# Optimization experiments

Hardware: AMD Instinct MI355X
Metric: run time of the kernel (lower is better)

The kernel has to match this reference:

```python
import jax, jax.numpy as jnp
import numpy as np

WEIGHT = 1.0  # init kwarg 'weight'


def _histc(x, bins):
    """torch.histc semantics: bins over [x.min(), x.max()], rightmost bin inclusive."""
    mn, mx = x.min(), x.max()
    w = (mx - mn) / bins
    safe_w = jnp.where(w > 0, w, 1.0)
    b = jnp.clip(jnp.floor((x - mn) / safe_w), 0, bins - 1).astype(jnp.int32)
    return jnp.zeros((bins,), jnp.float32).at[b].add(1.0)


def setup_inputs() -> dict:
    key = jax.random.key(0)
    k1, k2, k3 = jax.random.split(key, 3)
    C, H, W = 64, 128, 128
    inp = jax.random.normal(k1, (1, C, H, W), jnp.float32)
    match = jax.random.normal(k2, (1, C, H, W), jnp.float32)
    mask_tight = (jax.random.uniform(k3, (1, 1, H, W)) > 0.3).astype(jnp.float32)
    return {"input": inp, "match": match, "mask_tight": mask_tight, "bins": 256}


def reference(input, match, mask_tight, bins):
    C = input.shape[1]
    # --- compute_histogram (torch.histc per channel of masked match) ---
    mm = (match * mask_tight).reshape(C, -1)
    style_his = jax.lax.stop_gradient(jax.vmap(lambda v: _histc(v, bins))(mm))  # (C, bins)

    # --- remap_histogram ---
    x = (input * mask_tight).reshape(C, -1)  # (C, N)
    N = x.shape[1]
    channel_min = x.min(1, keepdims=True)  # (C,1)
    channel_max = x.max(1, keepdims=True)  # (C,1)
    step = (channel_max - channel_min) / bins
    rng = jnp.arange(1, N + 1, dtype=x.dtype)[None, :]  # (1, N) ranks 1..N

    sh = style_his * N / style_his.sum(1, keepdims=True)
    cdf = jnp.cumsum(sh, axis=1)                                  # (C, bins)
    cdf_prev = jnp.concatenate([jnp.zeros((C, 1), cdf.dtype), cdf[:, :-1]], axis=1)

    # CDF inversion: count bins whose cdf < rank  -> idx in [0, bins]
    idx = jnp.sum(cdf[:, None, :] - rng[:, :, None] < 0, axis=2).astype(jnp.int32)  # (C, N)

    # Faithful select_idx: gather from FLATTENED hist with un-offset bin indices
    flat_idx = idx.reshape(-1)
    sel = lambda h: h.reshape(-1)[flat_idx].reshape(C, N)

    ratio = jnp.clip((rng - sel(cdf_prev)) / (1e-8 + sel(cdf)), 0.0, 1.0)  # (C, N)
    input_corr = channel_min + (ratio + idx) * step
    input_corr = input_corr.at[:, -1].set(channel_max[:, 0])
    input_corr = sel(input_corr)  # faithful final flattened re-gather

    # --- loss (scalar stored as self.loss in the torch module) ---
    loss = jnp.mean((input_corr - x) ** 2)
    loss = loss * mask_tight.sum() * C / input.size * WEIGHT
    return loss
```

## Files before the change

### kernel.cpp

```cpp
#include <hip/hip_runtime.h>
#include <math.h>

#define C_CH  64
#define HW    16384
#define BINS  256

#define WS_CDF   0
#define WS_XMN   (C_CH * BINS)
#define WS_XMX   (WS_XMN + 1)
#define WS_MSUM  (WS_XMN + 2)
#define WS_SSE   (WS_XMN + 3)
#define WS_CNT   (WS_XMN + 4)

__device__ inline float4 ld4(const float* p) { return *(const float4*)p; }

__device__ inline int lbound(const float* a, float rank) {
    int lo = 0, hi = BINS;
    while (lo < hi) { int mid = (lo + hi) >> 1; if (a[mid] < rank) lo = mid + 1; else hi = mid; }
    return (lo > 255) ? 255 : lo;
}

__global__ __launch_bounds__(1024, 4) void k1_hist(const float* __restrict__ input,
                                                   const float* __restrict__ match,
                                                   const float* __restrict__ mask,
                                                   float* __restrict__ ws) {
    const int b = blockIdx.x, tid = threadIdx.x;
    const int wave = tid >> 6, lane = tid & 63;
    __shared__ float wmin[16], wmax[16], wsum[16];
    __shared__ int hist[BINS];

    if (b < C_CH) {
        const float* m = match + b * HW;

        float v[16];
        float mn = INFINITY, mx = -INFINITY;
        #pragma unroll
        for (int k = 0; k < 4; k++) {
            float4 mv = ld4(m + k * 4096 + 4 * tid);
            float4 kv = ld4(mask + k * 4096 + 4 * tid);
            v[4 * k + 0] = mv.x * kv.x; v[4 * k + 1] = mv.y * kv.y;
            v[4 * k + 2] = mv.z * kv.z; v[4 * k + 3] = mv.w * kv.w;
            #pragma unroll
            for (int j = 0; j < 4; j++) {
                mn = fminf(mn, v[4 * k + j]);
                mx = fmaxf(mx, v[4 * k + j]);
            }
        }
        #pragma unroll
        for (int s = 32; s > 0; s >>= 1) {
            mn = fminf(mn, __shfl_xor(mn, s, 64));
            mx = fmaxf(mx, __shfl_xor(mx, s, 64));
        }
        if (lane == 0) { wmin[wave] = mn; wmax[wave] = mx; }
        if (tid < BINS) hist[tid] = 0;
        __syncthreads();
        mn = wmin[0]; mx = wmax[0];
        #pragma unroll
        for (int j = 1; j < 16; j++) { mn = fminf(mn, wmin[j]); mx = fmaxf(mx, wmax[j]); }

        float w  = (mx - mn) * (1.0f / 256.0f);
        float sw = (w > 0.0f) ? w : 1.0f;

        int zc = 0;
        #pragma unroll
        for (int j = 0; j < 16; j++) {
            if (v[j] == 0.0f) { zc++; }
            else {
                float bb = floorf((v[j] - mn) / sw);
                bb = fminf(fmaxf(bb, 0.0f), 255.0f);
                atomicAdd(&hist[(int)bb], 1);
            }
        }
        #pragma unroll
        for (int s = 32; s > 0; s >>= 1) zc += __shfl_xor(zc, s, 64);
        if (lane == 0) wsum[wave] = (float)zc;
        __syncthreads();
        if (tid == 0) {
            int z = 0;
            #pragma unroll
            for (int j = 0; j < 16; j++) z += (int)wsum[j];
            float bb = floorf((0.0f - mn) / sw);
            bb = fminf(fmaxf(bb, 0.0f), 255.0f);
            hist[(int)bb] += z;
        }
        __syncthreads();

        if (wave == 0) {
            int h0 = hist[4 * lane], h1 = hist[4 * lane + 1];
            int h2 = hist[4 * lane + 2], h3 = hist[4 * lane + 3];
            int p1 = h0 + h1, p2 = p1 + h2, s4 = p2 + h3;
            int sc = s4;
            #pragma unroll
            for (int off = 1; off < 64; off <<= 1) {
                int t = __shfl_up(sc, off, 64);
                if (lane >= off) sc += t;
            }
            int e = sc - s4;
            float4 o = make_float4((float)(e + h0), (float)(e + p1),
                                   (float)(e + p2), (float)(e + s4));
            *(float4*)&ws[WS_CDF + b * BINS + 4 * lane] = o;
        }
    } else {
        float xmn = INFINITY, xmx = -INFINITY, msum = 0.0f;
        #pragma unroll
        for (int k = 0; k < 4; k++) {
            float4 xv = ld4(input + k * 4096 + 4 * tid);
            float4 kv = ld4(mask + k * 4096 + 4 * tid);
            float v0 = xv.x * kv.x, v1 = xv.y * kv.y, v2 = xv.z * kv.z, v3 = xv.w * kv.w;
            xmn = fminf(xmn, fminf(fminf(v0, v1), fminf(v2, v3)));
            xmx = fmaxf(xmx, fmaxf(fmaxf(v0, v1), fmaxf(v2, v3)));
            msum += kv.x + kv.y + kv.z + kv.w;
        }
        #pragma unroll
        for (int s = 32; s > 0; s >>= 1) {
            xmn = fminf(xmn, __shfl_xor(xmn, s, 64));
            xmx = fmaxf(xmx, __shfl_xor(xmx, s, 64));
            msum += __shfl_xor(msum, s, 64);
        }
        if (lane == 0) { wmin[wave] = xmn; wmax[wave] = xmx; wsum[wave] = msum; }
        __syncthreads();
        if (tid == 0) {
            #pragma unroll
            for (int j = 1; j < 16; j++) {
                xmn = fminf(xmn, wmin[j]);
                xmx = fmaxf(xmx, wmax[j]);
            }
            float ms = 0.0f;
            #pragma unroll
            for (int j = 0; j < 16; j++) ms += wsum[j];
            ws[WS_XMN] = xmn;
            ws[WS_XMX] = xmx;
            ws[WS_MSUM] = ms;
            ws[WS_SSE] = 0.0f;
            ((int*)ws)[WS_CNT] = 0;
        }
    }
}

__global__ __launch_bounds__(256) void k2_loss(const float* __restrict__ input,
                                               const float* __restrict__ mask,
                                               float* __restrict__ ws,
                                               float* __restrict__ out) {
    const int c = blockIdx.x >> 2;
    const int base = (blockIdx.x & 3) * 4096;
    const int tid = threadIdx.x;
    const int wave = tid >> 6, lane = tid & 63;

    __shared__ float scdf[BINS], sc0[BINS], sT[BINS], red[4];
    scdf[tid] = ws[WS_CDF + c * BINS + tid];
    sc0[tid]  = ws[WS_CDF + tid];
    __syncthreads();

    {
        const float xmn = ws[WS_XMN], xmx = ws[WS_XMX];
        float step = (xmx - xmn) * (1.0f / 256.0f);
        float rank = (float)(tid + 1);
        int idx = lbound(sc0, rank);
        float cp = (idx > 0) ? sc0[idx - 1] : 0.0f;
        float cc = sc0[idx];
        float ratio = fminf(fmaxf((rank - cp) / (1e-8f + cc), 0.0f), 1.0f);
        sT[tid] = xmn + (ratio + (float)idx) * step;
    }
    __syncthreads();

    const float* x  = input + c * HW + base;
    const float* mk = mask + base;

    float acc = 0.0f;
    int lo = lbound(scdf, (float)(base + 4 * tid + 1));
    #pragma unroll
    for (int k = 0; k < 4; k++) {
        float4 xv = ld4(x + k * 1024 + 4 * tid);
        float4 kv = ld4(mk + k * 1024 + 4 * tid);
        float v[4] = { xv.x * kv.x, xv.y * kv.y, xv.z * kv.z, xv.w * kv.w };
        float rank0 = (float)(base + k * 1024 + 4 * tid + 1);
        #pragma unroll
        for (int j = 0; j < 4; j++) {
            float rnk = rank0 + (float)j;
            while (scdf[lo] < rnk) lo++;
            float d = sT[lo] - v[j];
            acc += d * d;
        }
    }

    #pragma unroll
    for (int s = 32; s > 0; s >>= 1) acc += __shfl_xor(acc, s, 64);
    if (lane == 0) red[wave] = acc;
    __syncthreads();

    if (tid == 0) {
        float ssum = red[0] + red[1] + red[2] + red[3];
        atomicAdd(&ws[WS_SSE], ssum);
        __threadfence();
        int old = atomicAdd(&((int*)ws)[WS_CNT], 1);
        if (old == gridDim.x - 1) {
            float sse  = atomicAdd(&ws[WS_SSE], 0.0f);
            float msum = ws[WS_MSUM];
            double mean = (double)sse / (double)(C_CH * HW);
            out[0] = (float)(mean * (double)msum * (double)C_CH / (double)(C_CH * HW));
        }
    }
}

extern "C" void kernel_launch(void* const* d_in, const int* in_sizes, int n_in,
                              void* d_out, int out_size, void* d_ws, size_t ws_size,
                              hipStream_t stream) {
    const float* input = (const float*)d_in[0];
    const float* match = (const float*)d_in[1];
    const float* mask  = (const float*)d_in[2];
    float* ws          = (float*)d_ws;
    float* out         = (float*)d_out;

    k1_hist<<<C_CH + 1, 1024, 0, stream>>>(input, match, mask, ws);
    k2_loss<<<C_CH * 4, 256,  0, stream>>>(input, mask, ws, out);
}
```

Measured before the change: 78.91 us.

## Fuse histogram and loss kernels into one persistent kernel with grid barriers

Merges the two launches into a single 256-block kernel. Each block loads its quarter-channel slice of match, input and mask once and keeps the values in registers across phases. Software grid barriers synchronise the phases: partial min/max exchange, a per-block shared histogram merged into global with atomics, then CDF building and the loss. This removes a kernel launch and the second read of input, and spreads the histogram over four times more blocks. In exchange it relies on all 256 blocks being co-resident for the spin barriers and adds global atomic traffic.

```diff
diff --git a/kernel.cpp b/kernel.cpp
--- a/kernel.cpp
+++ b/kernel.cpp
@@ -4,15 +4,42 @@
 #define C_CH  64
 #define HW    16384
 #define BINS  256
-
-#define WS_CDF   0
-#define WS_XMN   (C_CH * BINS)
-#define WS_XMX   (WS_XMN + 1)
-#define WS_MSUM  (WS_XMN + 2)
-#define WS_SSE   (WS_XMN + 3)
-#define WS_CNT   (WS_XMN + 4)
+#define NBLK  256
+#define QHW   4096
+
+#define WS_HIST  0
+#define WS_PMIN  (C_CH * BINS)
+#define WS_PMAX  (WS_PMIN + C_CH * 4)
+#define WS_IPMN  (WS_PMAX + C_CH * 4)
+#define WS_IPMX  (WS_IPMN + 4)
+#define WS_MSUM  (WS_IPMX + 4)
+#define WS_SSE   (WS_MSUM + 4)
+#define WS_CNT   (WS_SSE + 1)
+
+__device__ unsigned g_bar_cnt = 0;
+__device__ unsigned g_bar_gen = 0;
 
 __device__ inline float4 ld4(const float* p) { return *(const float4*)p; }
+__device__ inline float aldf(float* p) { return atomicAdd(p, 0.0f); }
+__device__ inline int   aldi(int* p)   { return atomicAdd(p, 0); }
+
+__device__ inline void gridbar() {
+    __syncthreads();
+    if (threadIdx.x == 0) {
+        __threadfence();
+        unsigned g = __hip_atomic_load(&g_bar_gen, __ATOMIC_RELAXED, __HIP_MEMORY_SCOPE_AGENT);
+        if (atomicAdd(&g_bar_cnt, 1u) == NBLK - 1u) {
+            atomicExch(&g_bar_cnt, 0u);
+            __threadfence();
+            atomicAdd(&g_bar_gen, 1u);
+        } else {
+            while (__hip_atomic_load(&g_bar_gen, __ATOMIC_RELAXED, __HIP_MEMORY_SCOPE_AGENT) == g)
+                __builtin_amdgcn_s_sleep(1);
+        }
+        __threadfence();
+    }
+    __syncthreads();
+}
 
 __device__ inline int lbound(const float* a, float rank) {
     int lo = 0, hi = BINS;
@@ -20,184 +47,200 @@
     return (lo > 255) ? 255 : lo;
 }
 
-__global__ __launch_bounds__(1024, 4) void k1_hist(const float* __restrict__ input,
-                                                   const float* __restrict__ match,
-                                                   const float* __restrict__ mask,
-                                                   float* __restrict__ ws) {
-    const int b = blockIdx.x, tid = threadIdx.x;
+__global__ __launch_bounds__(256) void fused(const float* __restrict__ input,
+                                             const float* __restrict__ match,
+                                             const float* __restrict__ mask,
+                                             float* __restrict__ ws,
+                                             float* __restrict__ out) {
+    const int blk = blockIdx.x, tid = threadIdx.x;
+    const int c = blk >> 2, q = blk & 3, base = q * QHW;
     const int wave = tid >> 6, lane = tid & 63;
-    __shared__ float wmin[16], wmax[16], wsum[16];
-    __shared__ int hist[BINS];
-
-    if (b < C_CH) {
-        const float* m = match + b * HW;
-
-        float v[16];
-        float mn = INFINITY, mx = -INFINITY;
-        #pragma unroll
-        for (int k = 0; k < 4; k++) {
-            float4 mv = ld4(m + k * 4096 + 4 * tid);
-            float4 kv = ld4(mask + k * 4096 + 4 * tid);
-            v[4 * k + 0] = mv.x * kv.x; v[4 * k + 1] = mv.y * kv.y;
-            v[4 * k + 2] = mv.z * kv.z; v[4 * k + 3] = mv.w * kv.w;
+    int* iws = (int*)ws;
+
+    __shared__ int   hist[BINS];
+    __shared__ int   shc[BINS], sh0[BINS];
+    __shared__ float scdf[BINS], sc0[BINS], sT[BINS];
+    __shared__ float wr_a[4], wr_b[4], wr_c[4], wr_d[4], wr_e[4];
+    __shared__ float s_mn, s_mx, s_xmn, s_xmx;
+
+    const float* m  = match + c * HW + base;
+    const float* x  = input + c * HW + base;
+    const float* mk = mask + base;
+
+    float vm[16], vx[16];
+    float mn = INFINITY, mx = -INFINITY;
+    float xmn = INFINITY, xmx = -INFINITY, msum = 0.0f;
+    #pragma unroll
+    for (int k = 0; k < 4; k++) {
+        float4 mv = ld4(m  + k * 1024 + 4 * tid);
+        float4 kv = ld4(mk + k * 1024 + 4 * tid);
+        float4 xv = ld4(x  + k * 1024 + 4 * tid);
+        vm[4*k+0] = mv.x * kv.x; vm[4*k+1] = mv.y * kv.y;
+        vm[4*k+2] = mv.z * kv.z; vm[4*k+3] = mv.w * kv.w;
+        vx[4*k+0] = xv.x * kv.x; vx[4*k+1] = xv.y * kv.y;
+        vx[4*k+2] = xv.z * kv.z; vx[4*k+3] = xv.w * kv.w;
+        #pragma unroll
+        for (int j = 0; j < 4; j++) {
+            mn = fminf(mn, vm[4*k+j]);
+            mx = fmaxf(mx, vm[4*k+j]);
+        }
+        if (c == 0) {
             #pragma unroll
             for (int j = 0; j < 4; j++) {
-                mn = fminf(mn, v[4 * k + j]);
-                mx = fmaxf(mx, v[4 * k + j]);
+                xmn = fminf(xmn, vx[4*k+j]);
+                xmx = fmaxf(xmx, vx[4*k+j]);
             }
-        }
-        #pragma unroll
-        for (int s = 32; s > 0; s >>= 1) {
-            mn = fminf(mn, __shfl_xor(mn, s, 64));
-            mx = fmaxf(mx, __shfl_xor(mx, s, 64));
-        }
-        if (lane == 0) { wmin[wave] = mn; wmax[wave] = mx; }
-        if (tid < BINS) hist[tid] = 0;
-        __syncthreads();
-        mn = wmin[0]; mx = wmax[0];
-        #pragma unroll
-        for (int j = 1; j < 16; j++) { mn = fminf(mn, wmin[j]); mx = fmaxf(mx, wmax[j]); }
-
-        float w  = (mx - mn) * (1.0f / 256.0f);
-        float sw = (w > 0.0f) ? w : 1.0f;
-
-        int zc = 0;
-        #pragma unroll
-        for (int j = 0; j < 16; j++) {
-            if (v[j] == 0.0f) { zc++; }
-            else {
-                float bb = floorf((v[j] - mn) / sw);
-                bb = fminf(fmaxf(bb, 0.0f), 255.0f);
-                atomicAdd(&hist[(int)bb], 1);
-            }
-        }
-        #pragma unroll
-        for (int s = 32; s > 0; s >>= 1) zc += __shfl_xor(zc, s, 64);
-        if (lane == 0) wsum[wave] = (float)zc;
-        __syncthreads();
-        if (tid == 0) {
-            int z = 0;
-            #pragma unroll
-            for (int j = 0; j < 16; j++) z += (int)wsum[j];
-            float bb = floorf((0.0f - mn) / sw);
-            bb = fminf(fmaxf(bb, 0.0f), 255.0f);
-            hist[(int)bb] += z;
-        }
-        __syncthreads();
-
-        if (wave == 0) {
-            int h0 = hist[4 * lane], h1 = hist[4 * lane + 1];
-            int h2 = hist[4 * lane + 2], h3 = hist[4 * lane + 3];
-            int p1 = h0 + h1, p2 = p1 + h2, s4 = p2 + h3;
-            int sc = s4;
-            #pragma unroll
-            for (int off = 1; off < 64; off <<= 1) {
-                int t = __shfl_up(sc, off, 64);
-                if (lane >= off) sc += t;
-            }
-            int e = sc - s4;
-            float4 o = make_float4((float)(e + h0), (float)(e + p1),
-                                   (float)(e + p2), (float)(e + s4));
-            *(float4*)&ws[WS_CDF + b * BINS + 4 * lane] = o;
-        }
-    } else {
-        float xmn = INFINITY, xmx = -INFINITY, msum = 0.0f;
-        #pragma unroll
-        for (int k = 0; k < 4; k++) {
-            float4 xv = ld4(input + k * 4096 + 4 * tid);
-            float4 kv = ld4(mask + k * 4096 + 4 * tid);
-            float v0 = xv.x * kv.x, v1 = xv.y * kv.y, v2 = xv.z * kv.z, v3 = xv.w * kv.w;
-            xmn = fminf(xmn, fminf(fminf(v0, v1), fminf(v2, v3)));
-            xmx = fmaxf(xmx, fmaxf(fmaxf(v0, v1), fmaxf(v2, v3)));
             msum += kv.x + kv.y + kv.z + kv.w;
         }
+    }
+    #pragma unroll
+    for (int s = 32; s > 0; s >>= 1) {
+        mn = fminf(mn, __shfl_xor(mn, s, 64));
+        mx = fmaxf(mx, __shfl_xor(mx, s, 64));
+    }
+    if (c == 0) {
         #pragma unroll
         for (int s = 32; s > 0; s >>= 1) {
             xmn = fminf(xmn, __shfl_xor(xmn, s, 64));
             xmx = fmaxf(xmx, __shfl_xor(xmx, s, 64));
             msum += __shfl_xor(msum, s, 64);
         }
-        if (lane == 0) { wmin[wave] = xmn; wmax[wave] = xmx; wsum[wave] = msum; }
-        __syncthreads();
-        if (tid == 0) {
-            #pragma unroll
-            for (int j = 1; j < 16; j++) {
-                xmn = fminf(xmn, wmin[j]);
-                xmx = fmaxf(xmx, wmax[j]);
-            }
-            float ms = 0.0f;
-            #pragma unroll
-            for (int j = 0; j < 16; j++) ms += wsum[j];
-            ws[WS_XMN] = xmn;
-            ws[WS_XMX] = xmx;
-            ws[WS_MSUM] = ms;
-            ws[WS_SSE] = 0.0f;
-            ((int*)ws)[WS_CNT] = 0;
-        }
-    }
-}
-
-__global__ __launch_bounds__(256) void k2_loss(const float* __restrict__ input,
-                                               const float* __restrict__ mask,
-                                               float* __restrict__ ws,
-                                               float* __restrict__ out) {
-    const int c = blockIdx.x >> 2;
-    const int base = (blockIdx.x & 3) * 4096;
-    const int tid = threadIdx.x;
-    const int wave = tid >> 6, lane = tid & 63;
-
-    __shared__ float scdf[BINS], sc0[BINS], sT[BINS], red[4];
-    scdf[tid] = ws[WS_CDF + c * BINS + tid];
-    sc0[tid]  = ws[WS_CDF + tid];
+    }
+    if (lane == 0) {
+        wr_a[wave] = mn; wr_b[wave] = mx;
+        if (c == 0) { wr_c[wave] = msum; wr_d[wave] = xmn; wr_e[wave] = xmx; }
+    }
+    if (q == 0) atomicExch(&iws[WS_HIST + c * BINS + tid], 0);
+    if (blk == 0 && tid == 0) { atomicExch(&ws[WS_SSE], 0.0f); atomicExch(&iws[WS_CNT], 0); }
+    __syncthreads();
+    if (tid == 0) {
+        float a = wr_a[0], b = wr_b[0];
+        #pragma unroll
+        for (int j = 1; j < 4; j++) { a = fminf(a, wr_a[j]); b = fmaxf(b, wr_b[j]); }
+        atomicExch(&ws[WS_PMIN + c * 4 + q], a);
+        atomicExch(&ws[WS_PMAX + c * 4 + q], b);
+        if (c == 0) {
+            float ms  = wr_c[0] + wr_c[1] + wr_c[2] + wr_c[3];
+            float ixn = fminf(fminf(wr_d[0], wr_d[1]), fminf(wr_d[2], wr_d[3]));
+            float ixx = fmaxf(fmaxf(wr_e[0], wr_e[1]), fmaxf(wr_e[2], wr_e[3]));
+            atomicExch(&ws[WS_MSUM + q], ms);
+            atomicExch(&ws[WS_IPMN + q], ixn);
+            atomicExch(&ws[WS_IPMX + q], ixx);
+        }
+    }
+    gridbar();
+
+    if (tid == 0) {
+        float a = aldf(&ws[WS_PMIN + c * 4 + 0]);
+        float b = aldf(&ws[WS_PMAX + c * 4 + 0]);
+        #pragma unroll
+        for (int j = 1; j < 4; j++) {
+            a = fminf(a, aldf(&ws[WS_PMIN + c * 4 + j]));
+            b = fmaxf(b, aldf(&ws[WS_PMAX + c * 4 + j]));
+        }
+        s_mn = a; s_mx = b;
+    }
+    hist[tid] = 0;
+    __syncthreads();
+    mn = s_mn; mx = s_mx;
+
+    float w  = (mx - mn) * (1.0f / 256.0f);
+    float sw = (w > 0.0f) ? w : 1.0f;
+
+    int zc = 0;
+    #pragma unroll
+    for (int j = 0; j < 16; j++) {
+        if (vm[j] == 0.0f) { zc++; }
+        else {
+            float bb = floorf((vm[j] - mn) / sw);
+            bb = fminf(fmaxf(bb, 0.0f), 255.0f);
+            atomicAdd(&hist[(int)bb], 1);
+        }
+    }
+    #pragma unroll
+    for (int s = 32; s > 0; s >>= 1) zc += __shfl_xor(zc, s, 64);
+    if (lane == 0) wr_a[wave] = (float)zc;
+    __syncthreads();
+    if (tid == 0) {
+        int z = (int)wr_a[0] + (int)wr_a[1] + (int)wr_a[2] + (int)wr_a[3];
+        float bb = floorf((0.0f - mn) / sw);
+        bb = fminf(fmaxf(bb, 0.0f), 255.0f);
+        hist[(int)bb] += z;
+    }
+    __syncthreads();
+    atomicAdd(&iws[WS_HIST + c * BINS + tid], hist[tid]);
+    gridbar();
+
+    shc[tid] = aldi(&iws[WS_HIST + c * BINS + tid]);
+    sh0[tid] = (c == 0) ? shc[tid] : aldi(&iws[WS_HIST + tid]);
+    __syncthreads();
+    if (wave < 2) {
+        const int* hsrc = wave ? sh0 : shc;
+        float* dst = wave ? sc0 : scdf;
+        int h0 = hsrc[4*lane], h1 = hsrc[4*lane+1], h2 = hsrc[4*lane+2], h3 = hsrc[4*lane+3];
+        int p1 = h0 + h1, p2 = p1 + h2, s4 = p2 + h3;
+        int sc = s4;
+        #pragma unroll
+        for (int off = 1; off < 64; off <<= 1) {
+            int t = __shfl_up(sc, off, 64);
+            if (lane >= off) sc += t;
+        }
+        int e = sc - s4;
+        *(float4*)&dst[4*lane] = make_float4((float)(e + h0), (float)(e + p1),
+                                             (float)(e + p2), (float)(e + s4));
+    }
+    if (tid == 128) {
+        float a = aldf(&ws[WS_IPMN + 0]);
+        float b = aldf(&ws[WS_IPMX + 0]);
+        #pragma unroll
+        for (int j = 1; j < 4; j++) {
+            a = fminf(a, aldf(&ws[WS_IPMN + j]));
+            b = fmaxf(b, aldf(&ws[WS_IPMX + j]));
+        }
+        s_xmn = a; s_xmx = b;
+    }
     __syncthreads();
 
     {
-        const float xmn = ws[WS_XMN], xmx = ws[WS_XMX];
-        float step = (xmx - xmn) * (1.0f / 256.0f);
+        float step = (s_xmx - s_xmn) * (1.0f / 256.0f);
         float rank = (float)(tid + 1);
         int idx = lbound(sc0, rank);
         float cp = (idx > 0) ? sc0[idx - 1] : 0.0f;
         float cc = sc0[idx];
         float ratio = fminf(fmaxf((rank - cp) / (1e-8f + cc), 0.0f), 1.0f);
-        sT[tid] = xmn + (ratio + (float)idx) * step;
-    }
-    __syncthreads();
-
-    const float* x  = input + c * HW + base;
-    const float* mk = mask + base;
+        sT[tid] = s_xmn + (ratio + (float)idx) * step;
+    }
+    __syncthreads();
 
     float acc = 0.0f;
     int lo = lbound(scdf, (float)(base + 4 * tid + 1));
     #pragma unroll
     for (int k = 0; k < 4; k++) {
-        float4 xv = ld4(x + k * 1024 + 4 * tid);
-        float4 kv = ld4(mk + k * 1024 + 4 * tid);
-        float v[4] = { xv.x * kv.x, xv.y * kv.y, xv.z * kv.z, xv.w * kv.w };
         float rank0 = (float)(base + k * 1024 + 4 * tid + 1);
         #pragma unroll
         for (int j = 0; j < 4; j++) {
             float rnk = rank0 + (float)j;
             while (scdf[lo] < rnk) lo++;
-            float d = sT[lo] - v[j];
+            float d = sT[lo] - vx[4 * k + j];
             acc += d * d;
         }
     }
-
     #pragma unroll
     for (int s = 32; s > 0; s >>= 1) acc += __shfl_xor(acc, s, 64);
-    if (lane == 0) red[wave] = acc;
-    __syncthreads();
-
-    if (tid == 0) {
-        float ssum = red[0] + red[1] + red[2] + red[3];
+    if (lane == 0) wr_b[wave] = acc;
+    __syncthreads();
+
+    if (tid == 0) {
+        float ssum = wr_b[0] + wr_b[1] + wr_b[2] + wr_b[3];
         atomicAdd(&ws[WS_SSE], ssum);
         __threadfence();
-        int old = atomicAdd(&((int*)ws)[WS_CNT], 1);
-        if (old == gridDim.x - 1) {
-            float sse  = atomicAdd(&ws[WS_SSE], 0.0f);
-            float msum = ws[WS_MSUM];
+        int old = atomicAdd(&iws[WS_CNT], 1);
+        if (old == NBLK - 1) {
+            float sse = aldf(&ws[WS_SSE]);
+            float ms2 = aldf(&ws[WS_MSUM + 0]) + aldf(&ws[WS_MSUM + 1]) +
+                        aldf(&ws[WS_MSUM + 2]) + aldf(&ws[WS_MSUM + 3]);
             double mean = (double)sse / (double)(C_CH * HW);
-            out[0] = (float)(mean * (double)msum * (double)C_CH / (double)(C_CH * HW));
+            out[0] = (float)(mean * (double)ms2 * (double)C_CH / (double)(C_CH * HW));
         }
     }
 }
@@ -211,6 +254,5 @@
     float* ws          = (float*)d_ws;
     float* out         = (float*)d_out;
 
-    k1_hist<<<C_CH + 1, 1024, 0, stream>>>(input, match, mask, ws);
-    k2_loss<<<C_CH * 4, 256,  0, stream>>>(input, mask, ws, out);
-}
+    fused<<<NBLK, 256, 0, stream>>>(input, match, mask, ws, out);
+}
```

After: 142.3 us. 1.8x slower.

## Split histogram pipeline into three kernels with quarter-channel blocks

Applied to the files above, without the earlier changes.

The work is now split into more, smaller blocks. A new stats kernel computes per-quarter min and max (and the input stats from channel 0) across 256 blocks. The histogram kernel then builds per-quarter partial histograms across 256 blocks. The loss kernel sums these partials, rebuilds both CDFs in every block, and runs on 512 blocks with contiguous 8-element segments per thread. The aim is to use more of the GPU's compute units than the earlier 65 blocks of 1024 threads did. The cost is one extra kernel launch, re-reading the match data, and redundant CDF scans in every loss block.

```diff
diff --git a/kernel.cpp b/kernel.cpp
--- a/kernel.cpp
+++ b/kernel.cpp
@@ -4,15 +4,23 @@
 #define C_CH  64
 #define HW    16384
 #define BINS  256
-
-#define WS_CDF   0
-#define WS_XMN   (C_CH * BINS)
-#define WS_XMX   (WS_XMN + 1)
-#define WS_MSUM  (WS_XMN + 2)
-#define WS_SSE   (WS_XMN + 3)
-#define WS_CNT   (WS_XMN + 4)
+#define QHW   4096
+#define SEG   2048
+#define NB0   256
+#define NB1   256
+#define NB2   512
+
+#define WS_H     0
+#define WS_PMIN  (NB1 * BINS)
+#define WS_PMAX  (WS_PMIN + 256)
+#define WS_IPMN  (WS_PMAX + 256)
+#define WS_IPMX  (WS_IPMN + 4)
+#define WS_MSUM  (WS_IPMX + 4)
+#define WS_SSE   (WS_MSUM + 4)
+#define WS_CNT   (WS_SSE + 1)
 
 __device__ inline float4 ld4(const float* p) { return *(const float4*)p; }
+__device__ inline float aldf(float* p) { return atomicAdd(p, 0.0f); }
 
 __device__ inline int lbound(const float* a, float rank) {
     int lo = 0, hi = BINS;
@@ -20,50 +28,98 @@
     return (lo > 255) ? 255 : lo;
 }
 
-__global__ __launch_bounds__(1024, 4) void k1_hist(const float* __restrict__ input,
-                                                   const float* __restrict__ match,
-                                                   const float* __restrict__ mask,
-                                                   float* __restrict__ ws) {
-    const int b = blockIdx.x, tid = threadIdx.x;
+__global__ __launch_bounds__(256) void k0_stats(const float* __restrict__ input,
+                                                const float* __restrict__ match,
+                                                const float* __restrict__ mask,
+                                                float* __restrict__ ws) {
+    const int blk = blockIdx.x, tid = threadIdx.x;
+    const int c = blk >> 2, q = blk & 3;
     const int wave = tid >> 6, lane = tid & 63;
-    __shared__ float wmin[16], wmax[16], wsum[16];
+    __shared__ float wa[4], wb[4], wc[4], wd[4], we[4];
+
+    const float* m  = match + c * HW + q * QHW;
+    const float* mk = mask + q * QHW;
+
+    float mn = INFINITY, mx = -INFINITY;
+    float xmn = INFINITY, xmx = -INFINITY, ms = 0.0f;
+    #pragma unroll
+    for (int k = 0; k < 4; k++) {
+        float4 mv = ld4(m  + k * 1024 + 4 * tid);
+        float4 kv = ld4(mk + k * 1024 + 4 * tid);
+        float a0 = mv.x * kv.x, a1 = mv.y * kv.y, a2 = mv.z * kv.z, a3 = mv.w * kv.w;
+        mn = fminf(mn, fminf(fminf(a0, a1), fminf(a2, a3)));
+        mx = fmaxf(mx, fmaxf(fmaxf(a0, a1), fmaxf(a2, a3)));
+    }
+    if (c == 0) {
+        const float* x = input + q * QHW;
+        #pragma unroll
+        for (int k = 0; k < 4; k++) {
+            float4 xv = ld4(x  + k * 1024 + 4 * tid);
+            float4 kv = ld4(mk + k * 1024 + 4 * tid);
+            float b0 = xv.x * kv.x, b1 = xv.y * kv.y, b2 = xv.z * kv.z, b3 = xv.w * kv.w;
+            xmn = fminf(xmn, fminf(fminf(b0, b1), fminf(b2, b3)));
+            xmx = fmaxf(xmx, fmaxf(fmaxf(b0, b1), fmaxf(b2, b3)));
+            ms += kv.x + kv.y + kv.z + kv.w;
+        }
+    }
+    #pragma unroll
+    for (int s = 32; s > 0; s >>= 1) {
+        mn = fminf(mn, __shfl_xor(mn, s, 64));
+        mx = fmaxf(mx, __shfl_xor(mx, s, 64));
+        xmn = fminf(xmn, __shfl_xor(xmn, s, 64));
+        xmx = fmaxf(xmx, __shfl_xor(xmx, s, 64));
+        ms += __shfl_xor(ms, s, 64);
+    }
+    if (lane == 0) { wa[wave] = mn; wb[wave] = mx; wc[wave] = xmn; wd[wave] = xmx; we[wave] = ms; }
+    __syncthreads();
+    if (tid == 0) {
+        float a = wa[0], b = wb[0], cmin = wc[0], cmax = wd[0], msum = we[0];
+        #pragma unroll
+        for (int j = 1; j < 4; j++) {
+            a = fminf(a, wa[j]); b = fmaxf(b, wb[j]);
+            cmin = fminf(cmin, wc[j]); cmax = fmaxf(cmax, wd[j]); msum += we[j];
+        }
+        ws[WS_PMIN + c * 4 + q] = a;
+        ws[WS_PMAX + c * 4 + q] = b;
+        if (c == 0) {
+            ws[WS_IPMN + q] = cmin;
+            ws[WS_IPMX + q] = cmax;
+            ws[WS_MSUM + q] = msum;
+            if (q == 0) { ws[WS_SSE] = 0.0f; ((int*)ws)[WS_CNT] = 0; }
+        }
+    }
+}
+
+__global__ __launch_bounds__(256) void k1_hist(const float* __restrict__ match,
+                                               const float* __restrict__ mask,
+                                               float* __restrict__ ws) {
+    const int blk = blockIdx.x, tid = threadIdx.x;
+    const int c = blk >> 2, q = blk & 3;
+    const int wave = tid >> 6, lane = tid & 63;
     __shared__ int hist[BINS];
-
-    if (b < C_CH) {
-        const float* m = match + b * HW;
-
-        float v[16];
-        float mn = INFINITY, mx = -INFINITY;
-        #pragma unroll
-        for (int k = 0; k < 4; k++) {
-            float4 mv = ld4(m + k * 4096 + 4 * tid);
-            float4 kv = ld4(mask + k * 4096 + 4 * tid);
-            v[4 * k + 0] = mv.x * kv.x; v[4 * k + 1] = mv.y * kv.y;
-            v[4 * k + 2] = mv.z * kv.z; v[4 * k + 3] = mv.w * kv.w;
-            #pragma unroll
-            for (int j = 0; j < 4; j++) {
-                mn = fminf(mn, v[4 * k + j]);
-                mx = fmaxf(mx, v[4 * k + j]);
-            }
-        }
-        #pragma unroll
-        for (int s = 32; s > 0; s >>= 1) {
-            mn = fminf(mn, __shfl_xor(mn, s, 64));
-            mx = fmaxf(mx, __shfl_xor(mx, s, 64));
-        }
-        if (lane == 0) { wmin[wave] = mn; wmax[wave] = mx; }
-        if (tid < BINS) hist[tid] = 0;
-        __syncthreads();
-        mn = wmin[0]; mx = wmax[0];
-        #pragma unroll
-        for (int j = 1; j < 16; j++) { mn = fminf(mn, wmin[j]); mx = fmaxf(mx, wmax[j]); }
-
-        float w  = (mx - mn) * (1.0f / 256.0f);
-        float sw = (w > 0.0f) ? w : 1.0f;
-
-        int zc = 0;
-        #pragma unroll
-        for (int j = 0; j < 16; j++) {
+    __shared__ float wz[4];
+
+    float mn = fminf(fminf(ws[WS_PMIN + c * 4 + 0], ws[WS_PMIN + c * 4 + 1]),
+                     fminf(ws[WS_PMIN + c * 4 + 2], ws[WS_PMIN + c * 4 + 3]));
+    float mx = fmaxf(fmaxf(ws[WS_PMAX + c * 4 + 0], ws[WS_PMAX + c * 4 + 1]),
+                     fmaxf(ws[WS_PMAX + c * 4 + 2], ws[WS_PMAX + c * 4 + 3]));
+    hist[tid] = 0;
+    __syncthreads();
+
+    float w  = (mx - mn) * (1.0f / 256.0f);
+    float sw = (w > 0.0f) ? w : 1.0f;
+
+    const float* m  = match + c * HW + q * QHW;
+    const float* mk = mask + q * QHW;
+
+    int zc = 0;
+    #pragma unroll
+    for (int k = 0; k < 4; k++) {
+        float4 mv = ld4(m  + k * 1024 + 4 * tid);
+        float4 kv = ld4(mk + k * 1024 + 4 * tid);
+        float v[4] = { mv.x * kv.x, mv.y * kv.y, mv.z * kv.z, mv.w * kv.w };
+        #pragma unroll
+        for (int j = 0; j < 4; j++) {
             if (v[j] == 0.0f) { zc++; }
             else {
                 float bb = floorf((v[j] - mn) / sw);
@@ -71,95 +127,75 @@
                 atomicAdd(&hist[(int)bb], 1);
             }
         }
-        #pragma unroll
-        for (int s = 32; s > 0; s >>= 1) zc += __shfl_xor(zc, s, 64);
-        if (lane == 0) wsum[wave] = (float)zc;
-        __syncthreads();
-        if (tid == 0) {
-            int z = 0;
-            #pragma unroll
-            for (int j = 0; j < 16; j++) z += (int)wsum[j];
-            float bb = floorf((0.0f - mn) / sw);
-            bb = fminf(fmaxf(bb, 0.0f), 255.0f);
-            hist[(int)bb] += z;
-        }
-        __syncthreads();
-
-        if (wave == 0) {
-            int h0 = hist[4 * lane], h1 = hist[4 * lane + 1];
-            int h2 = hist[4 * lane + 2], h3 = hist[4 * lane + 3];
-            int p1 = h0 + h1, p2 = p1 + h2, s4 = p2 + h3;
-            int sc = s4;
-            #pragma unroll
-            for (int off = 1; off < 64; off <<= 1) {
-                int t = __shfl_up(sc, off, 64);
-                if (lane >= off) sc += t;
-            }
-            int e = sc - s4;
-            float4 o = make_float4((float)(e + h0), (float)(e + p1),
-                                   (float)(e + p2), (float)(e + s4));
-            *(float4*)&ws[WS_CDF + b * BINS + 4 * lane] = o;
-        }
-    } else {
-        float xmn = INFINITY, xmx = -INFINITY, msum = 0.0f;
-        #pragma unroll
-        for (int k = 0; k < 4; k++) {
-            float4 xv = ld4(input + k * 4096 + 4 * tid);
-            float4 kv = ld4(mask + k * 4096 + 4 * tid);
-            float v0 = xv.x * kv.x, v1 = xv.y * kv.y, v2 = xv.z * kv.z, v3 = xv.w * kv.w;
-            xmn = fminf(xmn, fminf(fminf(v0, v1), fminf(v2, v3)));
-            xmx = fmaxf(xmx, fmaxf(fmaxf(v0, v1), fmaxf(v2, v3)));
-            msum += kv.x + kv.y + kv.z + kv.w;
-        }
-        #pragma unroll
-        for (int s = 32; s > 0; s >>= 1) {
-            xmn = fminf(xmn, __shfl_xor(xmn, s, 64));
-            xmx = fmaxf(xmx, __shfl_xor(xmx, s, 64));
-            msum += __shfl_xor(msum, s, 64);
-        }
-        if (lane == 0) { wmin[wave] = xmn; wmax[wave] = xmx; wsum[wave] = msum; }
-        __syncthreads();
-        if (tid == 0) {
-            #pragma unroll
-            for (int j = 1; j < 16; j++) {
-                xmn = fminf(xmn, wmin[j]);
-                xmx = fmaxf(xmx, wmax[j]);
-            }
-            float ms = 0.0f;
-            #pragma unroll
-            for (int j = 0; j < 16; j++) ms += wsum[j];
-            ws[WS_XMN] = xmn;
-            ws[WS_XMX] = xmx;
-            ws[WS_MSUM] = ms;
-            ws[WS_SSE] = 0.0f;
-            ((int*)ws)[WS_CNT] = 0;
-        }
-    }
+    }
+    #pragma unroll
+    for (int s = 32; s > 0; s >>= 1) zc += __shfl_xor(zc, s, 64);
+    if (lane == 0) wz[wave] = (float)zc;
+    __syncthreads();
+    if (tid == 0) {
+        int z = (int)wz[0] + (int)wz[1] + (int)wz[2] + (int)wz[3];
+        float bb = floorf((0.0f - mn) / sw);
+        bb = fminf(fmaxf(bb, 0.0f), 255.0f);
+        hist[(int)bb] += z;
+    }
+    __syncthreads();
+    ((int*)ws)[WS_H + blk * BINS + tid] = hist[tid];
 }
 
 __global__ __launch_bounds__(256) void k2_loss(const float* __restrict__ input,
                                                const float* __restrict__ mask,
                                                float* __restrict__ ws,
                                                float* __restrict__ out) {
-    const int c = blockIdx.x >> 2;
-    const int base = (blockIdx.x & 3) * 4096;
-    const int tid = threadIdx.x;
+    const int blk = blockIdx.x, tid = threadIdx.x;
+    const int c = blk >> 3, s = blk & 7, base = s * SEG;
     const int wave = tid >> 6, lane = tid & 63;
-
+    int* iws = (int*)ws;
+
+    __shared__ int   shc[BINS], sh0[BINS];
     __shared__ float scdf[BINS], sc0[BINS], sT[BINS], red[4];
-    scdf[tid] = ws[WS_CDF + c * BINS + tid];
-    sc0[tid]  = ws[WS_CDF + tid];
-    __syncthreads();
+    __shared__ float s_xmn, s_xmx;
 
     {
-        const float xmn = ws[WS_XMN], xmx = ws[WS_XMX];
-        float step = (xmx - xmn) * (1.0f / 256.0f);
+        int h = iws[WS_H + (c * 4 + 0) * BINS + tid] + iws[WS_H + (c * 4 + 1) * BINS + tid]
+              + iws[WS_H + (c * 4 + 2) * BINS + tid] + iws[WS_H + (c * 4 + 3) * BINS + tid];
+        shc[tid] = h;
+        sh0[tid] = (c == 0) ? h
+                 : iws[WS_H + 0 * BINS + tid] + iws[WS_H + 1 * BINS + tid]
+                 + iws[WS_H + 2 * BINS + tid] + iws[WS_H + 3 * BINS + tid];
+    }
+    if (tid == 0) {
+        s_xmn = fminf(fminf(ws[WS_IPMN + 0], ws[WS_IPMN + 1]),
+                      fminf(ws[WS_IPMN + 2], ws[WS_IPMN + 3]));
+        s_xmx = fmaxf(fmaxf(ws[WS_IPMX + 0], ws[WS_IPMX + 1]),
+                      fmaxf(ws[WS_IPMX + 2], ws[WS_IPMX + 3]));
+    }
+    __syncthreads();
+
+    if (wave < 2) {
+        const int* hsrc = wave ? sh0 : shc;
+        float* dst = wave ? sc0 : scdf;
+        int h0 = hsrc[4*lane], h1 = hsrc[4*lane+1], h2 = hsrc[4*lane+2], h3 = hsrc[4*lane+3];
+        int p1 = h0 + h1, p2 = p1 + h2, s4 = p2 + h3;
+        int sc = s4;
+        #pragma unroll
+        for (int off = 1; off < 64; off <<= 1) {
+            int t = __shfl_up(sc, off, 64);
+            if (lane >= off) sc += t;
+        }
+        int e = sc - s4;
+        *(float4*)&dst[4*lane] = make_float4((float)(e + h0), (float)(e + p1),
+                                             (float)(e + p2), (float)(e + s4));
+    }
+    __syncthreads();
+
+    {
+        float step = (s_xmx - s_xmn) * (1.0f / 256.0f);
         float rank = (float)(tid + 1);
         int idx = lbound(sc0, rank);
         float cp = (idx > 0) ? sc0[idx - 1] : 0.0f;
         float cc = sc0[idx];
         float ratio = fminf(fmaxf((rank - cp) / (1e-8f + cc), 0.0f), 1.0f);
-        sT[tid] = xmn + (ratio + (float)idx) * step;
+        sT[tid] = s_xmn + (ratio + (float)idx) * step;
     }
     __syncthreads();
 
@@ -167,24 +203,23 @@
     const float* mk = mask + base;
 
     float acc = 0.0f;
-    int lo = lbound(scdf, (float)(base + 4 * tid + 1));
-    #pragma unroll
-    for (int k = 0; k < 4; k++) {
-        float4 xv = ld4(x + k * 1024 + 4 * tid);
-        float4 kv = ld4(mk + k * 1024 + 4 * tid);
+    const int r0 = base + 8 * tid + 1;
+    int lo = lbound(scdf, (float)r0);
+    #pragma unroll
+    for (int k = 0; k < 2; k++) {
+        float4 xv = ld4(x  + 8 * tid + 4 * k);
+        float4 kv = ld4(mk + 8 * tid + 4 * k);
         float v[4] = { xv.x * kv.x, xv.y * kv.y, xv.z * kv.z, xv.w * kv.w };
-        float rank0 = (float)(base + k * 1024 + 4 * tid + 1);
         #pragma unroll
         for (int j = 0; j < 4; j++) {
-            float rnk = rank0 + (float)j;
+            float rnk = (float)(r0 + 4 * k + j);
             while (scdf[lo] < rnk) lo++;
             float d = sT[lo] - v[j];
             acc += d * d;
         }
     }
-
-    #pragma unroll
-    for (int s = 32; s > 0; s >>= 1) acc += __shfl_xor(acc, s, 64);
+    #pragma unroll
+    for (int s2 = 32; s2 > 0; s2 >>= 1) acc += __shfl_xor(acc, s2, 64);
     if (lane == 0) red[wave] = acc;
     __syncthreads();
 
@@ -192,12 +227,12 @@
         float ssum = red[0] + red[1] + red[2] + red[3];
         atomicAdd(&ws[WS_SSE], ssum);
         __threadfence();
-        int old = atomicAdd(&((int*)ws)[WS_CNT], 1);
-        if (old == gridDim.x - 1) {
-            float sse  = atomicAdd(&ws[WS_SSE], 0.0f);
-            float msum = ws[WS_MSUM];
+        int old = atomicAdd(&iws[WS_CNT], 1);
+        if (old == NB2 - 1) {
+            float sse = aldf(&ws[WS_SSE]);
+            float ms2 = ws[WS_MSUM + 0] + ws[WS_MSUM + 1] + ws[WS_MSUM + 2] + ws[WS_MSUM + 3];
             double mean = (double)sse / (double)(C_CH * HW);
-            out[0] = (float)(mean * (double)msum * (double)C_CH / (double)(C_CH * HW));
+            out[0] = (float)(mean * (double)ms2 * (double)C_CH / (double)(C_CH * HW));
         }
     }
 }
@@ -211,6 +246,7 @@
     float* ws          = (float*)d_ws;
     float* out         = (float*)d_out;
 
-    k1_hist<<<C_CH + 1, 1024, 0, stream>>>(input, match, mask, ws);
-    k2_loss<<<C_CH * 4, 256,  0, stream>>>(input, mask, ws, out);
-}
+    k0_stats<<<NB0, 256, 0, stream>>>(input, match, mask, ws);
+    k1_hist<<<NB1, 256, 0, stream>>>(match, mask, ws);
+    k2_loss<<<NB2, 256, 0, stream>>>(input, mask, ws, out);
+}
```

After: 83.77 us. +6.2%, slower.

## Fuse histogram and loss kernels into one per-channel launch

Applied to the files above, without the earlier changes.

Merges the two kernels into a single 64-block kernel. Each block now also recomputes channel 0's histogram/CDF and the channel-0 input min/max plus the mask sum, so no workspace handoff between kernels is needed. The loss pass reads input values already held in registers, and each thread now handles 16 contiguous elements. In exchange it does redundant per-block loads and reductions, runs fewer blocks, and relies on self-resetting device globals for the final reduction.

```diff
diff --git a/kernel.cpp b/kernel.cpp
--- a/kernel.cpp
+++ b/kernel.cpp
@@ -5,12 +5,8 @@
 #define HW    16384
 #define BINS  256
 
-#define WS_CDF   0
-#define WS_XMN   (C_CH * BINS)
-#define WS_XMX   (WS_XMN + 1)
-#define WS_MSUM  (WS_XMN + 2)
-#define WS_SSE   (WS_XMN + 3)
-#define WS_CNT   (WS_XMN + 4)
+__device__ float    g_sse = 0.0f;
+__device__ unsigned g_cnt = 0u;
 
 __device__ inline float4 ld4(const float* p) { return *(const float4*)p; }
 
@@ -20,184 +16,175 @@
     return (lo > 255) ? 255 : lo;
 }
 
-__global__ __launch_bounds__(1024, 4) void k1_hist(const float* __restrict__ input,
-                                                   const float* __restrict__ match,
-                                                   const float* __restrict__ mask,
-                                                   float* __restrict__ ws) {
-    const int b = blockIdx.x, tid = threadIdx.x;
+__global__ __launch_bounds__(1024) void fused_one(const float* __restrict__ input,
+                                                  const float* __restrict__ match,
+                                                  const float* __restrict__ mask,
+                                                  float* __restrict__ out) {
+    const int c = blockIdx.x, tid = threadIdx.x;
     const int wave = tid >> 6, lane = tid & 63;
-    __shared__ float wmin[16], wmax[16], wsum[16];
-    __shared__ int hist[BINS];
-
-    if (b < C_CH) {
-        const float* m = match + b * HW;
-
-        float v[16];
-        float mn = INFINITY, mx = -INFINITY;
-        #pragma unroll
-        for (int k = 0; k < 4; k++) {
-            float4 mv = ld4(m + k * 4096 + 4 * tid);
-            float4 kv = ld4(mask + k * 4096 + 4 * tid);
-            v[4 * k + 0] = mv.x * kv.x; v[4 * k + 1] = mv.y * kv.y;
-            v[4 * k + 2] = mv.z * kv.z; v[4 * k + 3] = mv.w * kv.w;
-            #pragma unroll
-            for (int j = 0; j < 4; j++) {
-                mn = fminf(mn, v[4 * k + j]);
-                mx = fmaxf(mx, v[4 * k + j]);
-            }
-        }
-        #pragma unroll
-        for (int s = 32; s > 0; s >>= 1) {
-            mn = fminf(mn, __shfl_xor(mn, s, 64));
-            mx = fmaxf(mx, __shfl_xor(mx, s, 64));
-        }
-        if (lane == 0) { wmin[wave] = mn; wmax[wave] = mx; }
-        if (tid < BINS) hist[tid] = 0;
-        __syncthreads();
-        mn = wmin[0]; mx = wmax[0];
-        #pragma unroll
-        for (int j = 1; j < 16; j++) { mn = fminf(mn, wmin[j]); mx = fmaxf(mx, wmax[j]); }
-
-        float w  = (mx - mn) * (1.0f / 256.0f);
-        float sw = (w > 0.0f) ? w : 1.0f;
-
-        int zc = 0;
-        #pragma unroll
-        for (int j = 0; j < 16; j++) {
-            if (v[j] == 0.0f) { zc++; }
-            else {
-                float bb = floorf((v[j] - mn) / sw);
-                bb = fminf(fmaxf(bb, 0.0f), 255.0f);
-                atomicAdd(&hist[(int)bb], 1);
-            }
-        }
-        #pragma unroll
-        for (int s = 32; s > 0; s >>= 1) zc += __shfl_xor(zc, s, 64);
-        if (lane == 0) wsum[wave] = (float)zc;
-        __syncthreads();
-        if (tid == 0) {
-            int z = 0;
-            #pragma unroll
-            for (int j = 0; j < 16; j++) z += (int)wsum[j];
-            float bb = floorf((0.0f - mn) / sw);
-            bb = fminf(fmaxf(bb, 0.0f), 255.0f);
-            hist[(int)bb] += z;
-        }
-        __syncthreads();
-
-        if (wave == 0) {
-            int h0 = hist[4 * lane], h1 = hist[4 * lane + 1];
-            int h2 = hist[4 * lane + 2], h3 = hist[4 * lane + 3];
-            int p1 = h0 + h1, p2 = p1 + h2, s4 = p2 + h3;
-            int sc = s4;
-            #pragma unroll
-            for (int off = 1; off < 64; off <<= 1) {
-                int t = __shfl_up(sc, off, 64);
-                if (lane >= off) sc += t;
-            }
-            int e = sc - s4;
-            float4 o = make_float4((float)(e + h0), (float)(e + p1),
-                                   (float)(e + p2), (float)(e + s4));
-            *(float4*)&ws[WS_CDF + b * BINS + 4 * lane] = o;
-        }
-    } else {
-        float xmn = INFINITY, xmx = -INFINITY, msum = 0.0f;
-        #pragma unroll
-        for (int k = 0; k < 4; k++) {
-            float4 xv = ld4(input + k * 4096 + 4 * tid);
-            float4 kv = ld4(mask + k * 4096 + 4 * tid);
-            float v0 = xv.x * kv.x, v1 = xv.y * kv.y, v2 = xv.z * kv.z, v3 = xv.w * kv.w;
-            xmn = fminf(xmn, fminf(fminf(v0, v1), fminf(v2, v3)));
-            xmx = fmaxf(xmx, fmaxf(fmaxf(v0, v1), fmaxf(v2, v3)));
-            msum += kv.x + kv.y + kv.z + kv.w;
-        }
-        #pragma unroll
-        for (int s = 32; s > 0; s >>= 1) {
-            xmn = fminf(xmn, __shfl_xor(xmn, s, 64));
-            xmx = fmaxf(xmx, __shfl_xor(xmx, s, 64));
-            msum += __shfl_xor(msum, s, 64);
-        }
-        if (lane == 0) { wmin[wave] = xmn; wmax[wave] = xmx; wsum[wave] = msum; }
-        __syncthreads();
-        if (tid == 0) {
-            #pragma unroll
-            for (int j = 1; j < 16; j++) {
-                xmn = fminf(xmn, wmin[j]);
-                xmx = fmaxf(xmx, wmax[j]);
-            }
-            float ms = 0.0f;
-            #pragma unroll
-            for (int j = 0; j < 16; j++) ms += wsum[j];
-            ws[WS_XMN] = xmn;
-            ws[WS_XMX] = xmx;
-            ws[WS_MSUM] = ms;
-            ws[WS_SSE] = 0.0f;
-            ((int*)ws)[WS_CNT] = 0;
-        }
-    }
-}
-
-__global__ __launch_bounds__(256) void k2_loss(const float* __restrict__ input,
-                                               const float* __restrict__ mask,
-                                               float* __restrict__ ws,
-                                               float* __restrict__ out) {
-    const int c = blockIdx.x >> 2;
-    const int base = (blockIdx.x & 3) * 4096;
-    const int tid = threadIdx.x;
-    const int wave = tid >> 6, lane = tid & 63;
-
-    __shared__ float scdf[BINS], sc0[BINS], sT[BINS], red[4];
-    scdf[tid] = ws[WS_CDF + c * BINS + tid];
-    sc0[tid]  = ws[WS_CDF + tid];
-    __syncthreads();
-
-    {
-        const float xmn = ws[WS_XMN], xmx = ws[WS_XMX];
+
+    __shared__ int   hc[BINS], h0[BINS];
+    __shared__ float scdf[BINS], sc0[BINS], sT[BINS];
+    __shared__ float wr[7][16];
+
+    const float* mc = match + c * HW;
+    const float* xc = input + c * HW;
+    const int e0 = 16 * tid;
+
+    float vm[16], vm0[16], vx[16];
+    float mn = INFINITY,  mx = -INFINITY;
+    float mn0 = INFINITY, mx0 = -INFINITY;
+    float xmn = INFINITY, xmx = -INFINITY;
+    float ms = 0.0f;
+
+    #pragma unroll
+    for (int k = 0; k < 4; k++) {
+        float4 kv4 = ld4(mask  + e0 + 4 * k);
+        float4 a4  = ld4(mc    + e0 + 4 * k);
+        float4 b4  = ld4(match + e0 + 4 * k);
+        float4 c4  = ld4(xc    + e0 + 4 * k);
+        float4 d4  = ld4(input + e0 + 4 * k);
+        float kk[4] = { kv4.x, kv4.y, kv4.z, kv4.w };
+        float aa[4] = { a4.x, a4.y, a4.z, a4.w };
+        float bb[4] = { b4.x, b4.y, b4.z, b4.w };
+        float cc[4] = { c4.x, c4.y, c4.z, c4.w };
+        float dd[4] = { d4.x, d4.y, d4.z, d4.w };
+        #pragma unroll
+        for (int j = 0; j < 4; j++) {
+            float pm  = aa[j] * kk[j];
+            float pm0 = bb[j] * kk[j];
+            float px  = cc[j] * kk[j];
+            float p0  = dd[j] * kk[j];
+            vm [4*k+j] = pm;
+            vm0[4*k+j] = pm0;
+            vx [4*k+j] = px;
+            mn  = fminf(mn,  pm);  mx  = fmaxf(mx,  pm);
+            mn0 = fminf(mn0, pm0); mx0 = fmaxf(mx0, pm0);
+            xmn = fminf(xmn, p0);  xmx = fmaxf(xmx, p0);
+            ms += kk[j];
+        }
+    }
+    #pragma unroll
+    for (int s = 32; s > 0; s >>= 1) {
+        mn  = fminf(mn,  __shfl_xor(mn,  s, 64));
+        mx  = fmaxf(mx,  __shfl_xor(mx,  s, 64));
+        mn0 = fminf(mn0, __shfl_xor(mn0, s, 64));
+        mx0 = fmaxf(mx0, __shfl_xor(mx0, s, 64));
+        xmn = fminf(xmn, __shfl_xor(xmn, s, 64));
+        xmx = fmaxf(xmx, __shfl_xor(xmx, s, 64));
+        ms += __shfl_xor(ms, s, 64);
+    }
+    if (lane == 0) {
+        wr[0][wave] = mn;  wr[1][wave] = mx;
+        wr[2][wave] = mn0; wr[3][wave] = mx0;
+        wr[4][wave] = xmn; wr[5][wave] = xmx;
+        wr[6][wave] = ms;
+    }
+    if (tid < BINS) { hc[tid] = 0; h0[tid] = 0; }
+    __syncthreads();
+    mn = wr[0][0]; mx = wr[1][0]; mn0 = wr[2][0]; mx0 = wr[3][0];
+    xmn = wr[4][0]; xmx = wr[5][0]; ms = wr[6][0];
+    #pragma unroll
+    for (int j = 1; j < 16; j++) {
+        mn  = fminf(mn,  wr[0][j]); mx  = fmaxf(mx,  wr[1][j]);
+        mn0 = fminf(mn0, wr[2][j]); mx0 = fmaxf(mx0, wr[3][j]);
+        xmn = fminf(xmn, wr[4][j]); xmx = fmaxf(xmx, wr[5][j]);
+        ms += wr[6][j];
+    }
+
+    float swc = (mx  - mn ) * (1.0f / 256.0f); swc = (swc > 0.0f) ? swc : 1.0f;
+    float sw0 = (mx0 - mn0) * (1.0f / 256.0f); sw0 = (sw0 > 0.0f) ? sw0 : 1.0f;
+
+    int zc = 0, zc0 = 0;
+    #pragma unroll
+    for (int j = 0; j < 16; j++) {
+        if (vm[j] == 0.0f) { zc++; }
+        else {
+            float b = floorf((vm[j] - mn) / swc);
+            b = fminf(fmaxf(b, 0.0f), 255.0f);
+            atomicAdd(&hc[(int)b], 1);
+        }
+        if (vm0[j] == 0.0f) { zc0++; }
+        else {
+            float b = floorf((vm0[j] - mn0) / sw0);
+            b = fminf(fmaxf(b, 0.0f), 255.0f);
+            atomicAdd(&h0[(int)b], 1);
+        }
+    }
+    #pragma unroll
+    for (int s = 32; s > 0; s >>= 1) {
+        zc  += __shfl_xor(zc,  s, 64);
+        zc0 += __shfl_xor(zc0, s, 64);
+    }
+    if (lane == 0) { wr[0][wave] = (float)zc; wr[1][wave] = (float)zc0; }
+    __syncthreads();
+    if (tid == 0) {
+        int z = 0, z0 = 0;
+        #pragma unroll
+        for (int j = 0; j < 16; j++) { z += (int)wr[0][j]; z0 += (int)wr[1][j]; }
+        float b = floorf((0.0f - mn) / swc);
+        b = fminf(fmaxf(b, 0.0f), 255.0f);
+        hc[(int)b] += z;
+        float b0 = floorf((0.0f - mn0) / sw0);
+        b0 = fminf(fmaxf(b0, 0.0f), 255.0f);
+        h0[(int)b0] += z0;
+    }
+    __syncthreads();
+
+    if (wave < 2) {
+        const int* hsrc = wave ? h0 : hc;
+        float* dst = wave ? sc0 : scdf;
+        int a0 = hsrc[4*lane], a1 = hsrc[4*lane+1], a2 = hsrc[4*lane+2], a3 = hsrc[4*lane+3];
+        int p1 = a0 + a1, p2 = p1 + a2, s4 = p2 + a3;
+        int sc = s4;
+        #pragma unroll
+        for (int off = 1; off < 64; off <<= 1) {
+            int t = __shfl_up(sc, off, 64);
+            if (lane >= off) sc += t;
+        }
+        int e = sc - s4;
+        *(float4*)&dst[4*lane] = make_float4((float)(e + a0), (float)(e + p1),
+                                             (float)(e + p2), (float)(e + s4));
+    }
+    __syncthreads();
+    if (tid < BINS) {
         float step = (xmx - xmn) * (1.0f / 256.0f);
         float rank = (float)(tid + 1);
         int idx = lbound(sc0, rank);
         float cp = (idx > 0) ? sc0[idx - 1] : 0.0f;
-        float cc = sc0[idx];
-        float ratio = fminf(fmaxf((rank - cp) / (1e-8f + cc), 0.0f), 1.0f);
+        float cu = sc0[idx];
+        float ratio = fminf(fmaxf((rank - cp) / (1e-8f + cu), 0.0f), 1.0f);
         sT[tid] = xmn + (ratio + (float)idx) * step;
     }
     __syncthreads();
 
-    const float* x  = input + c * HW + base;
-    const float* mk = mask + base;
-
     float acc = 0.0f;
-    int lo = lbound(scdf, (float)(base + 4 * tid + 1));
-    #pragma unroll
-    for (int k = 0; k < 4; k++) {
-        float4 xv = ld4(x + k * 1024 + 4 * tid);
-        float4 kv = ld4(mk + k * 1024 + 4 * tid);
-        float v[4] = { xv.x * kv.x, xv.y * kv.y, xv.z * kv.z, xv.w * kv.w };
-        float rank0 = (float)(base + k * 1024 + 4 * tid + 1);
-        #pragma unroll
-        for (int j = 0; j < 4; j++) {
-            float rnk = rank0 + (float)j;
-            while (scdf[lo] < rnk) lo++;
-            float d = sT[lo] - v[j];
-            acc += d * d;
-        }
-    }
-
+    int lo = lbound(scdf, (float)(e0 + 1));
+    #pragma unroll
+    for (int i = 0; i < 16; i++) {
+        float rnk = (float)(e0 + i + 1);
+        while (scdf[lo] < rnk) lo++;
+        float d = sT[lo] - vx[i];
+        acc += d * d;
+    }
     #pragma unroll
     for (int s = 32; s > 0; s >>= 1) acc += __shfl_xor(acc, s, 64);
-    if (lane == 0) red[wave] = acc;
+    if (lane == 0) wr[0][wave] = acc;
     __syncthreads();
 
     if (tid == 0) {
-        float ssum = red[0] + red[1] + red[2] + red[3];
-        atomicAdd(&ws[WS_SSE], ssum);
+        float ssum = 0.0f;
+        #pragma unroll
+        for (int j = 0; j < 16; j++) ssum += wr[0][j];
+        atomicAdd(&g_sse, ssum);
         __threadfence();
-        int old = atomicAdd(&((int*)ws)[WS_CNT], 1);
-        if (old == gridDim.x - 1) {
-            float sse  = atomicAdd(&ws[WS_SSE], 0.0f);
-            float msum = ws[WS_MSUM];
+        unsigned old = atomicAdd(&g_cnt, 1u);
+        if (old == (unsigned)(C_CH - 1)) {
+            float sse = atomicAdd(&g_sse, 0.0f);
             double mean = (double)sse / (double)(C_CH * HW);
-            out[0] = (float)(mean * (double)msum * (double)C_CH / (double)(C_CH * HW));
+            out[0] = (float)(mean * (double)ms * (double)C_CH / (double)(C_CH * HW));
+            atomicExch(&g_sse, 0.0f);
+            atomicExch(&g_cnt, 0u);
         }
     }
 }
@@ -208,9 +195,8 @@
     const float* input = (const float*)d_in[0];
     const float* match = (const float*)d_in[1];
     const float* mask  = (const float*)d_in[2];
-    float* ws          = (float*)d_ws;
     float* out         = (float*)d_out;
-
-    k1_hist<<<C_CH + 1, 1024, 0, stream>>>(input, match, mask, ws);
-    k2_loss<<<C_CH * 4, 256,  0, stream>>>(input, mask, ws, out);
+    (void)d_ws; (void)ws_size;
+
+    fused_one<<<C_CH, 1024, 0, stream>>>(input, match, mask, out);
 }
```

Measured after the change: 84.01 us. +6.5%, slower.
